# Optimization experiments

Measured on AMD Instinct MI355X. Metric: run time of the kernel, lower is better.

## Reference

```python
import jax, jax.numpy as jnp
import numpy as np

DIM = 2048
NUM_HEADS = 16
NUM_KV_HEADS = 4
HEAD_DIM = DIM // NUM_HEADS  # 128
GROUP = NUM_HEADS // NUM_KV_HEADS  # queries per kv head
B, N = 2, 2048


def setup_inputs() -> dict:
    key = jax.random.key(0)
    ks = jax.random.split(key, 5)
    s = 1.0 / np.sqrt(DIM)
    return {
        "x": jax.random.normal(ks[0], (B, N, DIM), dtype=jnp.float32),
        "Wq": jax.random.normal(ks[1], (DIM, DIM), dtype=jnp.float32) * s,
        "Wk": jax.random.normal(ks[2], (DIM, NUM_KV_HEADS * HEAD_DIM), dtype=jnp.float32) * s,
        "Wv": jax.random.normal(ks[3], (DIM, NUM_KV_HEADS * HEAD_DIM), dtype=jnp.float32) * s,
        "Wo": jax.random.normal(ks[4], (DIM, DIM), dtype=jnp.float32) * s,
    }


def reference(x, Wq, Wk, Wv, Wo):
    Bc, Nc, C = x.shape
    scale = HEAD_DIM ** -0.5
    # projections -> [B, H, N, D] / [B, Hkv, N, D]
    q = (x @ Wq).reshape(Bc, Nc, NUM_HEADS, HEAD_DIM).transpose(0, 2, 1, 3)
    k = (x @ Wk).reshape(Bc, Nc, NUM_KV_HEADS, HEAD_DIM).transpose(0, 2, 1, 3)
    v = (x @ Wv).reshape(Bc, Nc, NUM_KV_HEADS, HEAD_DIM).transpose(0, 2, 1, 3)
    # repeat_interleave over head dim: kv head i serves query heads [i*G, (i+1)*G)
    k = jnp.repeat(k, GROUP, axis=1)  # [B, H, N, D]
    v = jnp.repeat(v, GROUP, axis=1)
    attn = jnp.einsum("bhqd,bhkd->bhqk", q, k) * scale
    attn = jax.nn.softmax(attn, axis=-1)
    out = jnp.einsum("bhqk,bhkd->bhqd", attn, v)  # [B, H, N, D]
    out = out.transpose(0, 2, 1, 3).reshape(Bc, Nc, C)
    return out @ Wo
```

## Files before the change

### kernel.cpp

```cpp
#include <hip/hip_runtime.h>
#include <hip/hip_bf16.h>
#include <cstdint>
#include <cstddef>

typedef __bf16 bf16;
typedef __attribute__((ext_vector_type(8))) __bf16 bf16x8;
typedef __attribute__((ext_vector_type(4))) float f32x4;
typedef __attribute__((ext_vector_type(16))) float f32x16;
typedef unsigned int u32;
typedef __attribute__((ext_vector_type(2))) unsigned int u32x2;

#define DEVINL __device__ __forceinline__

DEVINL void gload16(const void* g, void* l) {
  __builtin_amdgcn_global_load_lds(
      (const __attribute__((address_space(1))) void*)g,
      (__attribute__((address_space(3))) void*)l, 16, 0, 0);
}

DEVINL f32x4 mfma16(bf16x8 a, bf16x8 b, f32x4 c) {
  return __builtin_amdgcn_mfma_f32_16x16x32_bf16(a, b, c, 0, 0, 0);
}
DEVINL f32x16 mfma32(bf16x8 a, bf16x8 b, f32x16 c) {
  return __builtin_amdgcn_mfma_f32_32x32x16_bf16(a, b, c, 0, 0, 0);
}
DEVINL u32 cvtpk(float lo, float hi) {
  u32 r;
  asm("v_cvt_pk_bf16_f32 %0, %1, %2" : "=v"(r) : "v"(lo), "v"(hi));
  return r;
}
DEVINL void plswap(u32& a, u32& b) {
  asm("v_permlane32_swap_b32 %0, %1" : "+v"(a), "+v"(b));
}

__global__ __launch_bounds__(256) void cast_x_kernel(const float* __restrict__ x,
                                                     bf16* __restrict__ o, int n8) {
  int i = blockIdx.x * 256 + threadIdx.x;
  if (i >= n8) return;
  f32x4 a = ((const f32x4*)x)[2 * i];
  f32x4 b = ((const f32x4*)x)[2 * i + 1];
  bf16x8 v;
#pragma unroll
  for (int k = 0; k < 4; ++k) { v[k] = (bf16)a[k]; v[4 + k] = (bf16)b[k]; }
  ((bf16x8*)o)[i] = v;
}

__global__ __launch_bounds__(256) void transpose_cast_kernel(const float* __restrict__ src,
                                                             bf16* __restrict__ dst,
                                                             int K, int N) {
  __shared__ float tile[64][65];
  int nt = N >> 6;
  int n0 = (blockIdx.x % nt) << 6;
  int k0 = (blockIdx.x / nt) << 6;
  int c = threadIdx.x & 63, rb = threadIdx.x >> 6;
#pragma unroll
  for (int rr = 0; rr < 16; ++rr) {
    int row = rr * 4 + rb;
    tile[row][c] = src[(size_t)(k0 + row) * N + n0 + c];
  }
  __syncthreads();
#pragma unroll
  for (int rr = 0; rr < 16; ++rr) {
    int nrow = rr * 4 + rb;
    dst[(size_t)(n0 + nrow) * K + k0 + c] = (bf16)tile[c][nrow];
  }
}

template <int EPI>
__global__ __launch_bounds__(256) void gemm_bt_kernel(const bf16* __restrict__ A,
                                                      const bf16* __restrict__ BT,
                                                      float* __restrict__ Cout,
                                                      int Mtiles,
                                                      bf16* __restrict__ qb,
                                                      bf16* __restrict__ kb_,
                                                      bf16* __restrict__ vtb) {
  __shared__ __align__(16) unsigned char smem[16384];
  const int t = threadIdx.x, w = t >> 6, lane = t & 63;
  const int l4 = lane >> 4, l16 = lane & 15;
  const int bm = blockIdx.x % Mtiles, bn = blockIdx.x / Mtiles;
  const int wm = w >> 1, wn = w & 1;

  const char* aP[2];
  const char* bP[2];
#pragma unroll
  for (int p = 0; p < 2; ++p) {
    int g = p * 256 + t;
    aP[p] = (const char*)A + (size_t)(bm * 128 + (g >> 2)) * 4096 + (g & 3) * 16;
    bP[p] = (const char*)BT + (size_t)(bn * 128 + (g >> 2)) * 4096 + (g & 3) * 16;
  }
  const unsigned ldsW = w * 1024;

  const f32x4 fz = {0.f, 0.f, 0.f, 0.f};
  f32x4 acc[4][4];
#pragma unroll
  for (int i = 0; i < 4; ++i)
#pragma unroll
    for (int j = 0; j < 4; ++j) acc[i][j] = fz;

  const int arow = 64 * wm + l16, brow = 64 * wn + l16, kbyte = 16 * l4;

#pragma unroll 2
  for (int k0 = 0; k0 < 4096; k0 += 64) {
    gload16(aP[0] + k0, smem + ldsW);
    gload16(aP[1] + k0, smem + 4096 + ldsW);
    gload16(bP[0] + k0, smem + 8192 + ldsW);
    gload16(bP[1] + k0, smem + 12288 + ldsW);
    __syncthreads();
    bf16x8 af[4], bfr[4];
#pragma unroll
    for (int i = 0; i < 4; ++i)
      af[i] = *(const bf16x8*)(smem + (arow + 16 * i) * 64 + kbyte);
#pragma unroll
    for (int j = 0; j < 4; ++j)
      bfr[j] = *(const bf16x8*)(smem + 8192 + (brow + 16 * j) * 64 + kbyte);
#pragma unroll
    for (int i = 0; i < 4; ++i)
#pragma unroll
      for (int j = 0; j < 4; ++j)
        acc[i][j] = mfma16(af[i], bfr[j], acc[i][j]);
    __syncthreads();
  }

  const int r0 = bm * 128 + 64 * wm + 4 * l4;
  if (EPI == 1) {
#pragma unroll
    for (int j = 0; j < 4; ++j) {
      int col = bn * 128 + 64 * wn + 16 * j + l16;
#pragma unroll
      for (int i = 0; i < 4; ++i)
#pragma unroll
        for (int r = 0; r < 4; ++r)
          Cout[(size_t)(r0 + 16 * i + r) * 2048 + col] = acc[i][j][r];
    }
  } else {
    const int bq = bm >> 4;
#pragma unroll
    for (int j = 0; j < 4; ++j) {
      int col = bn * 128 + 64 * wn + 16 * j + l16;
      if (bn < 16) {
        int hh = col >> 7, d = col & 127;
        bf16* dst = qb + (size_t)((bq * 16 + hh) * 2048) * 128 + d;
#pragma unroll
        for (int i = 0; i < 4; ++i)
#pragma unroll
          for (int r = 0; r < 4; ++r) {
            int n = (r0 + 16 * i + r) & 2047;
            dst[(size_t)n * 128] = (bf16)acc[i][j][r];
          }
      } else if (bn < 20) {
        int kv = (col >> 7) - 16, d = col & 127;
        bf16* dst = kb_ + (size_t)((bq * 4 + kv) * 2048) * 128 + d;
#pragma unroll
        for (int i = 0; i < 4; ++i)
#pragma unroll
          for (int r = 0; r < 4; ++r) {
            int n = (r0 + 16 * i + r) & 2047;
            dst[(size_t)n * 128] = (bf16)acc[i][j][r];
          }
      } else {
        int kv = (col >> 7) - 20, d = col & 127;
        bf16* dst = vtb + ((size_t)(bq * 4 + kv) * 128 + d) * 2048;
#pragma unroll
        for (int i = 0; i < 4; ++i)
#pragma unroll
          for (int r = 0; r < 4; ++r) {
            int n = (r0 + 16 * i + r) & 2047;
            dst[n] = (bf16)acc[i][j][r];
          }
      }
    }
  }
}

__global__ __launch_bounds__(256, 2) void attn_kernel(const bf16* __restrict__ Q,
                                                      const bf16* __restrict__ K,
                                                      const bf16* __restrict__ VT,
                                                      bf16* __restrict__ AO) {
  __shared__ __align__(16) unsigned char smem[65536];
  const int t = threadIdx.x, w = t >> 6, lane = t & 63;
  const int q = lane & 31, hi = lane >> 5;
  const int pair = blockIdx.x >> 4;
  const int q00 = (blockIdx.x & 15) * 128 + w * 32;
  const int b = pair >> 4, h = pair & 15, kvh = h >> 2;
  const float KS2 = 0.08838834764831845f * 1.4426950408889634f;

  bf16x8 qf[8];
  {
    const char* qbase = (const char*)Q +
        ((size_t)((b * 16 + h) * 2048 + q00 + q) * 128 + 8 * hi) * 2;
#pragma unroll
    for (int dk = 0; dk < 8; ++dk) qf[dk] = *(const bf16x8*)(qbase + dk * 32);
  }

  f32x16 acc[4];
#pragma unroll
  for (int dt = 0; dt < 4; ++dt)
#pragma unroll
    for (int r = 0; r < 16; ++r) acc[dt][r] = 0.0f;
  float mrun = -1e30f, lrun = 0.0f;

  const char* Kg = (const char*)K + (size_t)((b * 4 + kvh) * 2048) * 256;
  const char* Vg = (const char*)VT + (size_t)((b * 4 + kvh) * 128) * 4096;

  auto STAGE = [&](unsigned base, int itn) {
    const int kb = itn * 64;
#pragma unroll
    for (int p = 0; p < 4; ++p) {
      int g = p * 256 + t;
      int row = g >> 4, cb = (g & 15) * 16;
      gload16(Kg + (size_t)(kb + row) * 256 + (cb ^ ((row & 7) << 4)),
              smem + base + p * 4096 + w * 1024);
    }
#pragma unroll
    for (int p = 0; p < 4; ++p) {
      int g = p * 256 + t;
      int row = g >> 3, cb = (g & 7) * 16;
      gload16(Vg + (size_t)row * 4096 + kb * 2 + (cb ^ ((row & 7) << 4)),
              smem + base + 16384 + p * 4096 + w * 1024);
    }
  };

  STAGE(0, 0);
  __syncthreads();

#pragma unroll 1
  for (int it = 0; it < 32; ++it) {
    const unsigned buf = (it & 1) ? 32768u : 0u;
    if (it < 31) STAGE(buf ^ 32768u, it + 1);

    f32x16 s0, s1;
#pragma unroll
    for (int r = 0; r < 16; ++r) { s0[r] = 0.0f; s1[r] = 0.0f; }
    __builtin_amdgcn_s_setprio(1);
#pragma unroll
    for (int dk = 0; dk < 8; ++dk) {
      const int cb = dk * 32 + 16 * hi;
      bf16x8 k0 = *(const bf16x8*)(smem + buf + q * 256 + (cb ^ ((q & 7) << 4)));
      bf16x8 k1 = *(const bf16x8*)(smem + buf + (q + 32) * 256 + (cb ^ ((q & 7) << 4)));
      s0 = mfma32(k0, qf[dk], s0);
      s1 = mfma32(k1, qf[dk], s1);
    }
    __builtin_amdgcn_s_setprio(0);

    float tm[16];
#pragma unroll
    for (int r = 0; r < 16; ++r) tm[r] = fmaxf(s0[r], s1[r]);
#pragma unroll
    for (int st = 8; st; st >>= 1)
#pragma unroll
      for (int r = 0; r < 8; ++r)
        if (r < st) tm[r] = fmaxf(tm[r], tm[r + st]);
    float mo = tm[0];
    mo = fmaxf(mo, __shfl_xor(mo, 32, 64));
    if (!__all((mo - mrun) * KS2 <= 8.0f)) {
      float mn = fmaxf(mrun, mo);
      float al = __builtin_amdgcn_exp2f((mrun - mn) * KS2);
      lrun *= al;
#pragma unroll
      for (int dt = 0; dt < 4; ++dt)
#pragma unroll
        for (int r = 0; r < 16; ++r) acc[dt][r] *= al;
      mrun = mn;
    }
    const float c0 = KS2 * mrun;
    float p0[16], p1[16];
#pragma unroll
    for (int r = 0; r < 16; ++r) {
      p0[r] = __builtin_amdgcn_exp2f(s0[r] * KS2 - c0);
      p1[r] = __builtin_amdgcn_exp2f(s1[r] * KS2 - c0);
    }
    float ts[16];
#pragma unroll
    for (int r = 0; r < 16; ++r) ts[r] = p0[r] + p1[r];
#pragma unroll
    for (int st = 8; st; st >>= 1)
#pragma unroll
      for (int r = 0; r < 8; ++r)
        if (r < st) ts[r] += ts[r + st];
    float rs = ts[0];
    rs += __shfl_xor(rs, 32, 64);
    lrun += rs;

    bf16x8 pa[4];
#pragma unroll
    for (int ks = 0; ks < 4; ++ks) {
      const int bs = (ks & 1) * 8;
      float* P = (ks >> 1) ? p1 : p0;
      u32 A0 = cvtpk(P[bs + 0], P[bs + 1]);
      u32 A1 = cvtpk(P[bs + 2], P[bs + 3]);
      u32 B0 = cvtpk(P[bs + 4], P[bs + 5]);
      u32 B1 = cvtpk(P[bs + 6], P[bs + 7]);
      plswap(A0, B0);
      plswap(A1, B1);
      union { u32 u[4]; bf16x8 v; } pu;
      pu.u[0] = A0; pu.u[1] = A1; pu.u[2] = B0; pu.u[3] = B1;
      pa[ks] = pu.v;
    }

    __builtin_amdgcn_s_setprio(1);
#pragma unroll
    for (int dt = 0; dt < 4; ++dt) {
      const int d = dt * 32 + q;
#pragma unroll
      for (int ks = 0; ks < 4; ++ks) {
        bf16x8 va = *(const bf16x8*)(smem + buf + 16384 + d * 128 +
                                     ((ks * 32 + 16 * hi) ^ ((d & 7) << 4)));
        acc[dt] = mfma32(va, pa[ks], acc[dt]);
      }
    }
    __builtin_amdgcn_s_setprio(0);
    __syncthreads();
  }

  const float inv = 1.0f / lrun;
  bf16* aorow = AO + (size_t)(b * 2048 + q00 + q) * 2048 + h * 128;
#pragma unroll
  for (int dt = 0; dt < 4; ++dt)
#pragma unroll
    for (int rq = 0; rq < 4; ++rq) {
      u32 w0 = cvtpk(acc[dt][rq * 4 + 0] * inv, acc[dt][rq * 4 + 1] * inv);
      u32 w1 = cvtpk(acc[dt][rq * 4 + 2] * inv, acc[dt][rq * 4 + 3] * inv);
      u32x2 pr; pr.x = w0; pr.y = w1;
      *(u32x2*)(aorow + dt * 32 + rq * 8 + 4 * hi) = pr;
    }
}

extern "C" void kernel_launch(void* const* d_in, const int* in_sizes, int n_in,
                              void* d_out, int out_size, void* d_ws, size_t ws_size,
                              hipStream_t stream) {
  const float* x = (const float*)d_in[0];
  const float* Wq = (const float*)d_in[1];
  const float* Wk = (const float*)d_in[2];
  const float* Wv = (const float*)d_in[3];
  const float* Wo = (const float*)d_in[4];

  char* ws = (char*)d_ws;
  bf16* xbf = (bf16*)(ws);
  bf16* WqkvT = (bf16*)(ws + 16777216);
  bf16* WoT = (bf16*)(ws + 29360128);
  bf16* Qbuf = (bf16*)(ws + 37748736);
  bf16* Kbuf = (bf16*)(ws + 54525952);
  bf16* VTbuf = (bf16*)(ws + 58720256);

  cast_x_kernel<<<4096, 256, 0, stream>>>(x, xbf, 1048576);
  transpose_cast_kernel<<<1024, 256, 0, stream>>>(Wq, WqkvT, 2048, 2048);
  transpose_cast_kernel<<<256, 256, 0, stream>>>(Wk, WqkvT + (size_t)2048 * 2048, 2048, 512);
  transpose_cast_kernel<<<256, 256, 0, stream>>>(Wv, WqkvT + (size_t)2560 * 2048, 2048, 512);
  transpose_cast_kernel<<<1024, 256, 0, stream>>>(Wo, WoT, 2048, 2048);

  gemm_bt_kernel<0><<<768, 256, 0, stream>>>(xbf, WqkvT, nullptr, 32, Qbuf, Kbuf, VTbuf);
  attn_kernel<<<512, 256, 0, stream>>>(Qbuf, Kbuf, VTbuf, xbf);
  gemm_bt_kernel<1><<<512, 256, 0, stream>>>(xbf, WoT, (float*)d_out, 32, nullptr, nullptr, nullptr);
}
```

Before: 216.5 us.

## Double-buffer GEMM LDS tiles and software-pipeline QK and PV in attention

The GEMM kernel now double-buffers its LDS tiles. The next k-slice is prefetched while the current one feeds the MFMAs, which removes one barrier per iteration. The attention kernel splits K and V staging and restructures the loop so that QK^T for tile i+1 runs alongside the softmax and PV work for tile i, using two sets of score registers. The cost is more LDS in both kernels and more registers in attention, which may lower occupancy.

```diff
diff --git a/kernel.cpp b/kernel.cpp
--- a/kernel.cpp
+++ b/kernel.cpp
@@ -74,7 +74,7 @@
                                                       bf16* __restrict__ qb,
                                                       bf16* __restrict__ kb_,
                                                       bf16* __restrict__ vtb) {
-  __shared__ __align__(16) unsigned char smem[16384];
+  __shared__ __align__(16) unsigned char smem[32768];
   const int t = threadIdx.x, w = t >> 6, lane = t & 63;
   const int l4 = lane >> 4, l16 = lane & 15;
   const int bm = blockIdx.x % Mtiles, bn = blockIdx.x / Mtiles;
@@ -90,6 +90,13 @@
   }
   const unsigned ldsW = w * 1024;
 
+  auto STAGE = [&](unsigned buf, int k0) {
+    gload16(aP[0] + k0, smem + buf * 16384 + ldsW);
+    gload16(aP[1] + k0, smem + buf * 16384 + 4096 + ldsW);
+    gload16(bP[0] + k0, smem + buf * 16384 + 8192 + ldsW);
+    gload16(bP[1] + k0, smem + buf * 16384 + 12288 + ldsW);
+  };
+
   const f32x4 fz = {0.f, 0.f, 0.f, 0.f};
   f32x4 acc[4][4];
 #pragma unroll
@@ -99,20 +106,20 @@
 
   const int arow = 64 * wm + l16, brow = 64 * wn + l16, kbyte = 16 * l4;
 
+  STAGE(0, 0);
+  __syncthreads();
+
 #pragma unroll 2
-  for (int k0 = 0; k0 < 4096; k0 += 64) {
-    gload16(aP[0] + k0, smem + ldsW);
-    gload16(aP[1] + k0, smem + 4096 + ldsW);
-    gload16(bP[0] + k0, smem + 8192 + ldsW);
-    gload16(bP[1] + k0, smem + 12288 + ldsW);
-    __syncthreads();
+  for (int tt = 0; tt < 64; ++tt) {
+    const unsigned buf = tt & 1;
+    if (tt < 63) STAGE(buf ^ 1u, (tt + 1) * 64);
     bf16x8 af[4], bfr[4];
 #pragma unroll
     for (int i = 0; i < 4; ++i)
-      af[i] = *(const bf16x8*)(smem + (arow + 16 * i) * 64 + kbyte);
+      af[i] = *(const bf16x8*)(smem + buf * 16384 + (arow + 16 * i) * 64 + kbyte);
 #pragma unroll
     for (int j = 0; j < 4; ++j)
-      bfr[j] = *(const bf16x8*)(smem + 8192 + (brow + 16 * j) * 64 + kbyte);
+      bfr[j] = *(const bf16x8*)(smem + buf * 16384 + 8192 + (brow + 16 * j) * 64 + kbyte);
 #pragma unroll
     for (int i = 0; i < 4; ++i)
 #pragma unroll
@@ -202,7 +209,8 @@
   const char* Kg = (const char*)K + (size_t)((b * 4 + kvh) * 2048) * 256;
   const char* Vg = (const char*)VT + (size_t)((b * 4 + kvh) * 128) * 4096;
 
-  auto STAGE = [&](unsigned base, int itn) {
+  auto STAGE_K = [&](int itn) {
+    const unsigned base = (unsigned)(itn & 1) * 16384u;
     const int kb = itn * 64;
 #pragma unroll
     for (int p = 0; p < 4; ++p) {
@@ -211,37 +219,36 @@
       gload16(Kg + (size_t)(kb + row) * 256 + (cb ^ ((row & 7) << 4)),
               smem + base + p * 4096 + w * 1024);
     }
+  };
+  auto STAGE_V = [&](int itn) {
+    const unsigned base = 32768u + (unsigned)(itn & 1) * 16384u;
+    const int kb = itn * 64;
 #pragma unroll
     for (int p = 0; p < 4; ++p) {
       int g = p * 256 + t;
       int row = g >> 3, cb = (g & 7) * 16;
       gload16(Vg + (size_t)row * 4096 + kb * 2 + (cb ^ ((row & 7) << 4)),
-              smem + base + 16384 + p * 4096 + w * 1024);
-    }
-  };
-
-  STAGE(0, 0);
-  __syncthreads();
-
-#pragma unroll 1
-  for (int it = 0; it < 32; ++it) {
-    const unsigned buf = (it & 1) ? 32768u : 0u;
-    if (it < 31) STAGE(buf ^ 32768u, it + 1);
-
-    f32x16 s0, s1;
+              smem + base + p * 4096 + w * 1024);
+    }
+  };
+
+  auto SMFMA = [&](int itn, f32x16& s0, f32x16& s1) {
+    const unsigned base = (unsigned)(itn & 1) * 16384u;
 #pragma unroll
     for (int r = 0; r < 16; ++r) { s0[r] = 0.0f; s1[r] = 0.0f; }
     __builtin_amdgcn_s_setprio(1);
 #pragma unroll
     for (int dk = 0; dk < 8; ++dk) {
       const int cb = dk * 32 + 16 * hi;
-      bf16x8 k0 = *(const bf16x8*)(smem + buf + q * 256 + (cb ^ ((q & 7) << 4)));
-      bf16x8 k1 = *(const bf16x8*)(smem + buf + (q + 32) * 256 + (cb ^ ((q & 7) << 4)));
+      bf16x8 k0 = *(const bf16x8*)(smem + base + q * 256 + (cb ^ ((q & 7) << 4)));
+      bf16x8 k1 = *(const bf16x8*)(smem + base + (q + 32) * 256 + (cb ^ ((q & 7) << 4)));
       s0 = mfma32(k0, qf[dk], s0);
       s1 = mfma32(k1, qf[dk], s1);
     }
     __builtin_amdgcn_s_setprio(0);
-
+  };
+
+  auto FINISH = [&](int itn, f32x16& s0, f32x16& s1) {
     float tm[16];
 #pragma unroll
     for (int r = 0; r < 16; ++r) tm[r] = fmaxf(s0[r], s1[r]);
@@ -297,20 +304,49 @@
       pa[ks] = pu.v;
     }
 
+    const unsigned vbase = 32768u + (unsigned)(itn & 1) * 16384u;
     __builtin_amdgcn_s_setprio(1);
 #pragma unroll
     for (int dt = 0; dt < 4; ++dt) {
       const int d = dt * 32 + q;
 #pragma unroll
       for (int ks = 0; ks < 4; ++ks) {
-        bf16x8 va = *(const bf16x8*)(smem + buf + 16384 + d * 128 +
+        bf16x8 va = *(const bf16x8*)(smem + vbase + d * 128 +
                                      ((ks * 32 + 16 * hi) ^ ((d & 7) << 4)));
         acc[dt] = mfma32(va, pa[ks], acc[dt]);
       }
     }
     __builtin_amdgcn_s_setprio(0);
+  };
+
+  f32x16 sA0, sA1, sB0, sB1;
+  STAGE_K(0);
+  __syncthreads();
+
+  STAGE_K(1);
+  STAGE_V(0);
+  SMFMA(0, sA0, sA1);
+  __syncthreads();
+
+#pragma unroll 1
+  for (int i = 1; i < 31; i += 2) {
+    STAGE_K(i + 1);
+    STAGE_V(i);
+    SMFMA(i, sB0, sB1);
+    FINISH(i - 1, sA0, sA1);
     __syncthreads();
-  }
+    STAGE_K(i + 2);
+    STAGE_V(i + 1);
+    SMFMA(i + 1, sA0, sA1);
+    FINISH(i, sB0, sB1);
+    __syncthreads();
+  }
+
+  STAGE_V(31);
+  SMFMA(31, sB0, sB1);
+  FINISH(30, sA0, sA1);
+  __syncthreads();
+  FINISH(31, sB0, sB1);
 
   const float inv = 1.0f / lrun;
   bf16* aorow = AO + (size_t)(b * 2048 + q00 + q) * 2048 + h * 128;
```

Result: no change. 213.4 us (-1.4%).
